# Optimization experiments

Measured on AMD Instinct MI355X. Metric: run time of the kernel, lower is better.

Reference implementation:

```python
import jax, jax.numpy as jnp
import numpy as np

N = 131072          # flattened ray-sample points
C = 32              # output_coordinate_dim per plane
BASE = 128          # base grid resolution
SCALES = [1, 2, 4]  # multiscale_res multipliers
HID = 256           # ResBlock / CondMLP hidden width
OUT = 16            # decoder output dim (geo features)
COMBS = [(0, 1), (0, 2), (1, 2)]  # itertools.combinations(range(3), 2)


def setup_inputs() -> dict:
    key = jax.random.key(0)
    ks = iter(jax.random.split(key, 64))
    inp = {}
    inp['pts'] = jax.random.uniform(next(ks), (N, 3), dtype=jnp.float32)
    inp['aabb'] = jnp.asarray([[0.0, 0.0, 0.0], [1.0, 1.0, 1.0]], dtype=jnp.float32)
    # 9 plane grids: 3 scales x 3 coordinate combinations, uniform in [0.1, 0.5)
    for s, mult in enumerate(SCALES):
        r = BASE * mult
        for ci in range(3):
            inp[f'plane_{s}_{ci}'] = jax.random.uniform(
                next(ks), (C, r, r), dtype=jnp.float32, minval=0.1, maxval=0.5)
    feat_dim = C * len(SCALES)  # concat across scales -> 96
    def lin(k, fin, fout):
        bound = 1.0 / np.sqrt(fin)
        kw, kb = jax.random.split(k)
        w = jax.random.uniform(kw, (fin, fout), dtype=jnp.float32, minval=-bound, maxval=bound)
        b = jax.random.uniform(kb, (fout,), dtype=jnp.float32, minval=-bound, maxval=bound)
        return w, b
    inp['l0_w'], inp['l0_b'] = lin(next(ks), feat_dim, HID)
    # 3 ResBlocks x 3 linears (lz, l1, l2), all 256x256 -> stacked
    rw, rb = [], []
    for _ in range(9):
        w, b = lin(next(ks), HID, HID)
        rw.append(w); rb.append(b)
    inp['res_w'] = jnp.stack(rw).reshape(3, 3, HID, HID)
    inp['res_b'] = jnp.stack(rb).reshape(3, 3, HID)
    inp['l1_w'], inp['l1_b'] = lin(next(ks), HID, OUT)
    return inp


def _bilinear(plane, xy):
    # plane: [C, H, W]; xy: [N, 2] in [-1, 1]; x -> W axis, y -> H axis
    # (F.grid_sample, align_corners=True; border clamp == zeros pad since pts in-bounds)
    Cc, H, W = plane.shape
    x = (xy[:, 0] + 1.0) * 0.5 * (W - 1)
    y = (xy[:, 1] + 1.0) * 0.5 * (H - 1)
    x0 = jnp.clip(jnp.floor(x), 0, W - 2).astype(jnp.int32)
    y0 = jnp.clip(jnp.floor(y), 0, H - 2).astype(jnp.int32)
    x1, y1 = x0 + 1, y0 + 1
    wx = (x - x0)[None, :]
    wy = (y - y0)[None, :]
    v = (plane[:, y0, x0] * (1 - wx) * (1 - wy)
         + plane[:, y0, x1] * wx * (1 - wy)
         + plane[:, y1, x0] * (1 - wx) * wy
         + plane[:, y1, x1] * wx * wy)          # [C, N]
    return v.T                                   # [N, C]


def _interp_ms(xn, planes):
    # planes: list of 3 scales, each a list of 3 [C,H,W] grids
    feats = []
    for scale_planes in planes:
        interp = 1.0
        for plane, (c0, c1) in zip(scale_planes, COMBS):
            xy = jnp.stack([xn[:, c0], xn[:, c1]], axis=-1)
            interp = interp * _bilinear(plane, xy)  # hadamard across planes
        feats.append(interp)
    return jnp.concatenate(feats, axis=-1)          # [N, C*num_scales]


def _cond_mlp(f, l0_w, l0_b, res_w, res_b, l1_w, l1_b):
    x = f @ l0_w + l0_b
    for i in range(3):
        z = jax.nn.relu(x @ res_w[i, 0] + res_b[i, 0])
        res = x + z
        x = jax.nn.relu(res @ res_w[i, 1] + res_b[i, 1])
        x = jax.nn.relu(x @ res_w[i, 2] + res_b[i, 2]) + res
    return jax.nn.sigmoid(x @ l1_w + l1_b)


def reference(pts, aabb,
              plane_0_0, plane_0_1, plane_0_2,
              plane_1_0, plane_1_1, plane_1_2,
              plane_2_0, plane_2_1, plane_2_2,
              l0_w, l0_b, res_w, res_b, l1_w, l1_b):
    xn = (pts - aabb[0]) * (2.0 / (aabb[1] - aabb[0])) - 1.0  # normalize_aabb
    planes = [[plane_0_0, plane_0_1, plane_0_2],
              [plane_1_0, plane_1_1, plane_1_2],
              [plane_2_0, plane_2_1, plane_2_2]]
    feats = _interp_ms(xn, planes)                            # [N, 96]
    return _cond_mlp(feats, l0_w, l0_b, res_w, res_b, l1_w, l1_b)  # [N, 16]
```

## Files before the change

### kernel.cpp

```cpp
#include <hip/hip_runtime.h>

typedef unsigned short u16;
typedef unsigned int u32;
typedef __attribute__((ext_vector_type(2))) unsigned int u32x2;
typedef __attribute__((ext_vector_type(4))) unsigned int u32x4;
typedef __attribute__((ext_vector_type(8))) short short8;
typedef __attribute__((ext_vector_type(8))) _Float16 half8;
typedef __attribute__((ext_vector_type(2))) __fp16 fp16x2;
typedef __attribute__((ext_vector_type(4))) float floatx4;

__device__ __forceinline__ u16 f2h(float f){ _Float16 h = (_Float16)f; return __builtin_bit_cast(u16, h); }
__device__ __forceinline__ u32 pkrtz(float a, float b){
  fp16x2 h = __builtin_amdgcn_cvt_pkrtz(a, b);
  return __builtin_bit_cast(u32, h);
}
__device__ __forceinline__ u32 pkmax0(u32 a){
  u32 d, z = 0;
  asm("v_pk_max_f16 %0, %1, %2" : "=v"(d) : "v"(a), "v"(z));
  return d;
}
__device__ __forceinline__ u32 pkadd(u32 a, u32 b){
  u32 d;
  asm("v_pk_add_f16 %0, %1, %2" : "=v"(d) : "v"(a), "v"(b));
  return d;
}
__device__ __forceinline__ u32 pkmul(u32 a, u32 b){
  u32 d;
  asm("v_pk_mul_f16 %0, %1, %2" : "=v"(d) : "v"(a), "v"(b));
  return d;
}
__device__ __forceinline__ u32 pkfma(u32 a, u32 b, u32 c){
  u32 d;
  asm("v_pk_fma_f16 %0, %1, %2, %3" : "=v"(d) : "v"(a), "v"(b), "v"(c));
  return d;
}

struct PlanePtrs { const void* p[9]; };
struct PtransArgs { const float* src[9]; u16* dst[9]; int blk0[10]; int HW[9]; };

__global__ void ptrans_all_kernel(PtransArgs a){
  __shared__ float tile[32][257];
  int bi = blockIdx.x;
  int i = 0;
  #pragma unroll
  for (int k = 1; k < 9; k++) if (bi >= a.blk0[k]) i = k;
  const float* src = a.src[i];
  u16* dst = a.dst[i];
  const int HW = a.HW[i];
  const int t = threadIdx.x;
  const size_t hw0 = (size_t)(bi - a.blk0[i]) * 256;
  #pragma unroll
  for (int c = 0; c < 32; c++) tile[c][t] = src[(size_t)c*HW + hw0 + t];
  __syncthreads();
  u32* d32 = (u32*)(dst + hw0*32);
  #pragma unroll
  for (int k = 0; k < 16; k++){
    int idx = k*512 + t*2;
    int j = idx >> 5, cc = idx & 31;
    u32 lo = f2h(tile[cc][j]);
    u32 hi = f2h(tile[cc+1][j]);
    d32[k*256 + t] = lo | (hi << 16);
  }
}

__device__ __forceinline__ void wconv_one(const float* src, u16* dst, int fin, int fout, int t){
  int per = fin * fout;
  int m = t / per, r = t - m*per;
  int KS = fin >> 5;
  int e = r & 7;
  int lane = (r >> 3) & 63;
  int fs = r >> 9;
  int ks = fs % KS, ft = fs / KS;
  int of = ft*16 + (lane & 15);
  int k  = ks*32 + (lane >> 4)*8 + e;
  dst[t] = f2h(src[(size_t)m*per + (size_t)k*fout + of]);
}
__global__ void wconv_all_kernel(const float* l0_w, const float* res_w, const float* l1_w,
                                 u16* l0T, u16* resT, u16* l1T){
  int t = blockIdx.x*256 + threadIdx.x;
  if (t < 24576){ wconv_one(l0_w, l0T, 96, 256, t); return; }
  t -= 24576;
  if (t < 589824){ wconv_one(res_w, resT, 256, 256, t); return; }
  t -= 589824;
  if (t < 4096){ wconv_one(l1_w, l1T, 256, 16, t); }
}

__device__ __forceinline__ u32 morton_key(const float* __restrict__ pts,
                                          const float* __restrict__ aabb, int n){
  u32 key = 0;
  #pragma unroll
  for (int d=0; d<3; d++){
    float lo = aabb[d], hi = aabb[3+d];
    float xn = (pts[(size_t)n*3 + d] - lo) * (2.0f/(hi - lo)) - 1.0f;
    int q = (int)((xn + 1.0f) * 8.0f);
    q = q < 0 ? 0 : (q > 15 ? 15 : q);
    #pragma unroll
    for (int b=0; b<4; b++) key |= ((u32)(q >> b) & 1u) << (b*3 + d);
  }
  return key;
}
__global__ void hist_kernel(const float* pts, const float* aabb, u32* hist, int N){
  int n = blockIdx.x*256 + threadIdx.x;
  if (n >= N) return;
  atomicAdd(&hist[morton_key(pts, aabb, n)], 1u);
}
__global__ void scan_kernel(u32* hist){
  __shared__ u32 sums[1024];
  int t = threadIdx.x;
  u32 local[4]; u32 s = 0;
  #pragma unroll
  for (int i=0; i<4; i++){ local[i] = hist[t*4 + i]; s += local[i]; }
  sums[t] = s;
  __syncthreads();
  for (int off=1; off<1024; off<<=1){
    u32 v = (t >= off) ? sums[t-off] : 0;
    __syncthreads();
    sums[t] += v;
    __syncthreads();
  }
  u32 base = (t == 0) ? 0 : sums[t-1];
  #pragma unroll
  for (int i=0; i<4; i++){ u32 c = local[i]; hist[t*4 + i] = base; base += c; }
}
__global__ void scatter_kernel(const float* pts, const float* aabb, u32* hist,
                               int* sidx, int N){
  int n = blockIdx.x*256 + threadIdx.x;
  if (n >= N) return;
  u32 pos = atomicAdd(&hist[morton_key(pts, aabb, n)], 1u);
  sidx[pos] = n;
}

__global__ void interp_fb_kernel(const float* __restrict__ pts, const float* __restrict__ aabb,
                                 PlanePtrs pp, u16* __restrict__ feats, int N)
{
  int n = blockIdx.x*256 + threadIdx.x;
  if (n >= N) return;
  float xn[3];
  #pragma unroll
  for (int d=0; d<3; d++){
    float lo = aabb[d], hi = aabb[3+d];
    xn[d] = (pts[(size_t)n*3 + d] - lo) * (2.0f/(hi - lo)) - 1.0f;
  }
  const int c0s[3] = {0,0,1};
  const int c1s[3] = {1,2,2};
  #pragma unroll
  for (int s=0; s<3; s++){
    const int R = 128 << s;
    float prod[32];
    #pragma unroll
    for (int p=0; p<3; p++){
      float fx = (xn[c0s[p]] + 1.0f) * 0.5f * (float)(R-1);
      float fy = (xn[c1s[p]] + 1.0f) * 0.5f * (float)(R-1);
      float fx0 = fminf(fmaxf(floorf(fx), 0.0f), (float)(R-2));
      float fy0 = fminf(fmaxf(floorf(fy), 0.0f), (float)(R-2));
      int x0 = (int)fx0, y0 = (int)fy0;
      float wx = fx - fx0, wy = fy - fy0;
      float w00 = (1.0f-wx)*(1.0f-wy), w01 = wx*(1.0f-wy);
      float w10 = (1.0f-wx)*wy,        w11 = wx*wy;
      const size_t HW = (size_t)R*R;
      const float* b00f = (const float*)pp.p[s*3+p] + (size_t)y0*R + x0;
      #pragma unroll 4
      for (int c=0; c<32; c++){
        const float* q = b00f + (size_t)c*HW;
        float val = q[0]*w00 + q[1]*w01 + q[R]*w10 + q[R+1]*w11;
        prod[c] = (p == 0) ? val : prod[c]*val;
      }
    }
    #pragma unroll
    for (int vv=0; vv<4; vv++){
      short8 pk8;
      #pragma unroll
      for (int e=0; e<8; e++) pk8[e] = (short)f2h(prod[vv*8+e]);
      *(short8*)(feats + (size_t)n*96 + s*32 + vv*8) = pk8;
    }
  }
}

template<int KSTEPS>
__device__ __forceinline__ void mm_tile(const u16* X, const u16* __restrict__ WTs,
                                        int ftbase, int lane, floatx4 acc[4][4])
{
  const int lr = lane & 15, lg = lane >> 4;
  const u16* wbase = WTs + (size_t)lane*8;
  half8 wc[4];
  #pragma unroll
  for (int rf=0; rf<4; rf++)
    wc[rf] = *(const half8*)(wbase + (size_t)((ftbase+rf)*KSTEPS)*512);
  #pragma unroll 2
  for (int ks=0; ks<KSTEPS; ks++){
    half8 x[4];
    #pragma unroll
    for (int cf=0; cf<4; cf++){
      int pt = cf*16 + lr;
      int byt = (pt*512 + (ks*32 + lg*8)*2) ^ ((pt & 31) << 4);
      x[cf] = *(const half8*)((const char*)X + byt);
    }
    half8 wn[4];
    {
      int ksn = (ks+1 < KSTEPS) ? ks+1 : ks;
      #pragma unroll
      for (int rf=0; rf<4; rf++)
        wn[rf] = *(const half8*)(wbase + (size_t)((ftbase+rf)*KSTEPS + ksn)*512);
    }
    __builtin_amdgcn_s_setprio(1);
    #pragma unroll
    for (int rf=0; rf<4; rf++)
      #pragma unroll
      for (int cf=0; cf<4; cf++)
        acc[rf][cf] = __builtin_amdgcn_mfma_f32_16x16x32_f16(wc[rf], x[cf], acc[rf][cf], 0, 0, 0);
    __builtin_amdgcn_s_setprio(0);
    #pragma unroll
    for (int rf=0; rf<4; rf++) wc[rf] = wn[rf];
  }
}

__device__ __forceinline__ void init_acc(const float* b, int wb, int lg, floatx4 acc[4][4]){
  #pragma unroll
  for (int rf=0; rf<4; rf++){
    float4 v = *(const float4*)(b + wb + rf*16 + lg*4);
    floatx4 bi = (floatx4){v.x, v.y, v.z, v.w};
    #pragma unroll
    for (int cf=0; cf<4; cf++) acc[rf][cf] = bi;
  }
}

template<int MODE>
__global__ __launch_bounds__(256, 3) void mlp_kernel(
    const float* __restrict__ pts, const float* __restrict__ aabb, PlanePtrs pp,
    const u16* __restrict__ feats, const int* __restrict__ sidx,
    const u16* __restrict__ l0T, const u16* __restrict__ resT, const u16* __restrict__ l1T,
    const float* __restrict__ l0_b, const float* __restrict__ res_b, const float* __restrict__ l1_b,
    float* __restrict__ out)
{
  __shared__ u16 X[64*256];
  const int tid = threadIdx.x;
  const int wave = tid >> 6, lane = tid & 63;
  const int lr = lane & 15, lg = lane >> 4;
  int bid = blockIdx.x;
  if constexpr (MODE == 2){
    int nwg = gridDim.x;
    if ((nwg & 7) == 0) bid = (bid & 7)*(nwg >> 3) + (bid >> 3);
  }
  const int n0 = bid * 64;
  const int ftbase = wave * 4;
  const int wb = wave * 64;

  if constexpr (MODE >= 1){
    const int pt = tid >> 2, v = tid & 3;
    const int n = (MODE == 2) ? sidx[n0 + pt] : (n0 + pt);
    float xn[3];
    #pragma unroll
    for (int d=0; d<3; d++){
      float lo = aabb[d], hi = aabb[3+d];
      xn[d] = (pts[(size_t)n*3 + d] - lo) * (2.0f/(hi - lo)) - 1.0f;
    }
    const int c0s[3] = {0,0,1};
    const int c1s[3] = {1,2,2};
    #pragma unroll
    for (int s=0; s<3; s++){
      const int R = 128 << s;
      u32x4 prod;
      #pragma unroll
      for (int p=0; p<3; p++){
        float fx = (xn[c0s[p]] + 1.0f) * 0.5f * (float)(R-1);
        float fy = (xn[c1s[p]] + 1.0f) * 0.5f * (float)(R-1);
        float fx0 = fminf(fmaxf(floorf(fx), 0.0f), (float)(R-2));
        float fy0 = fminf(fmaxf(floorf(fy), 0.0f), (float)(R-2));
        int x0 = (int)fx0, y0 = (int)fy0;
        float wx = fx - fx0, wy = fy - fy0;
        u32 w00p = pkrtz((1.0f-wx)*(1.0f-wy), (1.0f-wx)*(1.0f-wy));
        u32 w01p = pkrtz(wx*(1.0f-wy),        wx*(1.0f-wy));
        u32 w10p = pkrtz((1.0f-wx)*wy,        (1.0f-wx)*wy);
        u32 w11p = pkrtz(wx*wy,               wx*wy);
        const u16* base = (const u16*)pp.p[s*3 + p];
        const u16* b00 = base + ((size_t)y0*R + x0)*32 + v*8;
        const u16* b10 = b00 + (size_t)R*32;
        u32x4 h00 = *(const u32x4*)b00;
        u32x4 h01 = *(const u32x4*)(b00 + 32);
        u32x4 h10 = *(const u32x4*)b10;
        u32x4 h11 = *(const u32x4*)(b10 + 32);
        #pragma unroll
        for (int i=0; i<4; i++){
          u32 a = pkmul(h00[i], w00p);
          a = pkfma(h01[i], w01p, a);
          a = pkfma(h10[i], w10p, a);
          a = pkfma(h11[i], w11p, a);
          prod[i] = (p == 0) ? a : pkmul(prod[i], a);
        }
      }
      int byt = (pt*512 + (s*32 + v*8)*2) ^ ((pt & 31) << 4);
      *(u32x4*)((char*)X + byt) = prod;
    }
  } else {
    #pragma unroll
    for (int i=0; i<3; i++){
      int id = tid + i*256;
      int row = id / 12, sub = id - row*12;
      short8 v = *(const short8*)(feats + (size_t)(n0+row)*96 + sub*8);
      int byt = (row*512 + sub*16) ^ ((row & 31) << 4);
      *(short8*)((char*)X + byt) = v;
    }
  }
  __syncthreads();

  floatx4 acc[4][4];
  u32 pk[4][4][2];

  init_acc(l0_b, wb, lg, acc);
  mm_tile<3>(X, l0T, ftbase, lane, acc);
  __syncthreads();
  #pragma unroll
  for (int rf=0; rf<4; rf++){
    int fby = (wb + rf*16 + lg*4)*2;
    #pragma unroll
    for (int cf=0; cf<4; cf++){
      int pt = cf*16 + lr;
      u32 p0 = pkrtz(acc[rf][cf][0], acc[rf][cf][1]);
      u32 p1 = pkrtz(acc[rf][cf][2], acc[rf][cf][3]);
      pk[rf][cf][0] = p0; pk[rf][cf][1] = p1;
      int byt = (pt*512 + fby) ^ ((pt & 31) << 4);
      *(u32x2*)((char*)X + byt) = (u32x2){p0, p1};
    }
  }
  __syncthreads();

  for (int rb=0; rb<3; rb++){
    const u16* W0 = resT + (size_t)(rb*3+0)*65536;
    const u16* W1 = resT + (size_t)(rb*3+1)*65536;
    const u16* W2 = resT + (size_t)(rb*3+2)*65536;
    const float* b0 = res_b + (rb*3+0)*256;
    const float* b1 = res_b + (rb*3+1)*256;
    const float* b2 = res_b + (rb*3+2)*256;

    init_acc(b0, wb, lg, acc);
    mm_tile<8>(X, W0, ftbase, lane, acc);
    __syncthreads();
    #pragma unroll
    for (int rf=0; rf<4; rf++){
      int fby = (wb + rf*16 + lg*4)*2;
      #pragma unroll
      for (int cf=0; cf<4; cf++){
        int pt = cf*16 + lr;
        u32 p0 = pkadd(pk[rf][cf][0], pkmax0(pkrtz(acc[rf][cf][0], acc[rf][cf][1])));
        u32 p1 = pkadd(pk[rf][cf][1], pkmax0(pkrtz(acc[rf][cf][2], acc[rf][cf][3])));
        pk[rf][cf][0] = p0; pk[rf][cf][1] = p1;
        int byt = (pt*512 + fby) ^ ((pt & 31) << 4);
        *(u32x2*)((char*)X + byt) = (u32x2){p0, p1};
      }
    }
    __syncthreads();

    init_acc(b1, wb, lg, acc);
    mm_tile<8>(X, W1, ftbase, lane, acc);
    __syncthreads();
    #pragma unroll
    for (int rf=0; rf<4; rf++){
      int fby = (wb + rf*16 + lg*4)*2;
      #pragma unroll
      for (int cf=0; cf<4; cf++){
        int pt = cf*16 + lr;
        u32 p0 = pkmax0(pkrtz(acc[rf][cf][0], acc[rf][cf][1]));
        u32 p1 = pkmax0(pkrtz(acc[rf][cf][2], acc[rf][cf][3]));
        int byt = (pt*512 + fby) ^ ((pt & 31) << 4);
        *(u32x2*)((char*)X + byt) = (u32x2){p0, p1};
      }
    }
    __syncthreads();

    init_acc(b2, wb, lg, acc);
    mm_tile<8>(X, W2, ftbase, lane, acc);
    __syncthreads();
    #pragma unroll
    for (int rf=0; rf<4; rf++){
      int fby = (wb + rf*16 + lg*4)*2;
      #pragma unroll
      for (int cf=0; cf<4; cf++){
        int pt = cf*16 + lr;
        u32 p0 = pkadd(pkmax0(pkrtz(acc[rf][cf][0], acc[rf][cf][1])), pk[rf][cf][0]);
        u32 p1 = pkadd(pkmax0(pkrtz(acc[rf][cf][2], acc[rf][cf][3])), pk[rf][cf][1]);
        pk[rf][cf][0] = p0; pk[rf][cf][1] = p1;
        int byt = (pt*512 + fby) ^ ((pt & 31) << 4);
        *(u32x2*)((char*)X + byt) = (u32x2){p0, p1};
      }
    }
    __syncthreads();
  }

  floatx4 accf;
  {
    float4 bo = *(const float4*)(l1_b + lg*4);
    accf = (floatx4){bo.x, bo.y, bo.z, bo.w};
  }
  #pragma unroll 1
  for (int ks=0; ks<8; ks++){
    int pt = wave*16 + lr;
    int byt = (pt*512 + (ks*32 + lg*8)*2) ^ ((pt&31)<<4);
    half8 x = *(const half8*)((const char*)X + byt);
    half8 w = *(const half8*)(l1T + ((size_t)ks*64 + lane)*8);
    accf = __builtin_amdgcn_mfma_f32_16x16x32_f16(w, x, accf, 0, 0, 0);
  }
  {
    int li = n0 + wave*16 + lr;
    int n_out = (MODE == 2) ? sidx[li] : li;
    float4 o;
    o.x = 1.0f / (1.0f + __expf(-accf[0]));
    o.y = 1.0f / (1.0f + __expf(-accf[1]));
    o.z = 1.0f / (1.0f + __expf(-accf[2]));
    o.w = 1.0f / (1.0f + __expf(-accf[3]));
    *(float4*)(out + (size_t)n_out*16 + lg*4) = o;
  }
}

extern "C" void kernel_launch(void* const* d_in, const int* in_sizes, int n_in,
                              void* d_out, int out_size, void* d_ws, size_t ws_size,
                              hipStream_t stream)
{
  const float* pts  = (const float*)d_in[0];
  const float* aabb = (const float*)d_in[1];
  const float* l0_w = (const float*)d_in[11];
  const float* res_w= (const float*)d_in[13];
  const float* l1_w = (const float*)d_in[15];
  const float* l0_b = (const float*)d_in[12];
  const float* res_b= (const float*)d_in[14];
  const float* l1_b = (const float*)d_in[16];
  const int N = in_sizes[0] / 3;

  char* ws = (char*)d_ws;
  const size_t woff_l0  = 0;
  const size_t woff_res = 49152;
  const size_t woff_l1  = woff_res + 9*65536*2;
  const size_t foff     = woff_l1 + 8192;
  const size_t poff     = foff + (size_t)N*96*2;

  static const int HWs[3] = {128*128, 256*256, 512*512};
  size_t pel[9]; size_t tot = 0;
  for (int s=0;s<3;s++) for (int p=0;p<3;p++){ pel[s*3+p] = tot; tot += (size_t)HWs[s]*32; }

  const size_t hoff = (poff + tot*2 + 255) & ~(size_t)255;
  const size_t ioff = hoff + 4096*4;
  const bool tr_mode   = (ws_size >= poff + tot*2);
  const bool sort_mode = (ws_size >= ioff + (size_t)N*4) && ((N/64) % 8 == 0) && (N % 256 == 0);

  wconv_all_kernel<<<(24576+589824+4096+255)/256, 256, 0, stream>>>(
      l0_w, res_w, l1_w, (u16*)(ws+woff_l0), (u16*)(ws+woff_res), (u16*)(ws+woff_l1));

  PlanePtrs pp;
  if (tr_mode){
    u16* pbase = (u16*)(ws + poff);
    PtransArgs pa;
    int b0 = 0;
    for (int i=0;i<9;i++){
      int s = i/3;
      pa.src[i] = (const float*)d_in[2+i];
      pa.dst[i] = pbase + pel[i];
      pa.blk0[i] = b0;
      pa.HW[i] = HWs[s];
      b0 += HWs[s]/256;
      pp.p[i] = pbase + pel[i];
    }
    pa.blk0[9] = b0;
    ptrans_all_kernel<<<b0, 256, 0, stream>>>(pa);

    if (sort_mode){
      u32* hist = (u32*)(ws + hoff);
      int* sidx = (int*)(ws + ioff);
      hipMemsetAsync(hist, 0, 4096*4, stream);
      hist_kernel<<<(N+255)/256, 256, 0, stream>>>(pts, aabb, hist, N);
      scan_kernel<<<1, 1024, 0, stream>>>(hist);
      scatter_kernel<<<(N+255)/256, 256, 0, stream>>>(pts, aabb, hist, sidx, N);
      mlp_kernel<2><<<N/64, 256, 0, stream>>>(pts, aabb, pp, (const u16*)nullptr, sidx,
          (const u16*)(ws+woff_l0), (const u16*)(ws+woff_res), (const u16*)(ws+woff_l1),
          l0_b, res_b, l1_b, (float*)d_out);
    } else {
      mlp_kernel<1><<<N/64, 256, 0, stream>>>(pts, aabb, pp, (const u16*)nullptr, (const int*)nullptr,
          (const u16*)(ws+woff_l0), (const u16*)(ws+woff_res), (const u16*)(ws+woff_l1),
          l0_b, res_b, l1_b, (float*)d_out);
    }
  } else {
    for (int i=0;i<9;i++) pp.p[i] = d_in[2+i];
    interp_fb_kernel<<<(N+255)/256, 256, 0, stream>>>(pts, aabb, pp, (u16*)(ws+foff), N);
    mlp_kernel<0><<<N/64, 256, 0, stream>>>(pts, aabb, pp, (const u16*)(ws+foff), (const int*)nullptr,
        (const u16*)(ws+woff_l0), (const u16*)(ws+woff_res), (const u16*)(ws+woff_l1),
        l0_b, res_b, l1_b, (float*)d_out);
  }
}
```

Baseline: 269.7 us.

## Drop Morton sort path, merge prep kernels, simplify weight loading in MFMA loop

Removes the Morton-order histogram/scan/scatter sorting and the sorted-index indirection in the MLP kernel, so points are processed in natural order. The plane-transpose and weight-conversion kernels are merged into one launch. The MFMA inner loop stops software-prefetching next-step weights and stops unrolling, loading weights in the same step instead. This cuts four launches and the sort overhead, but may lose the gather locality that sorting gave to plane sampling and expose weight-load latency in the GEMM loop.

```diff
diff --git a/kernel.cpp b/kernel.cpp
--- a/kernel.cpp
+++ b/kernel.cpp
@@ -36,32 +36,12 @@
 }
 
 struct PlanePtrs { const void* p[9]; };
-struct PtransArgs { const float* src[9]; u16* dst[9]; int blk0[10]; int HW[9]; };
-
-__global__ void ptrans_all_kernel(PtransArgs a){
-  __shared__ float tile[32][257];
-  int bi = blockIdx.x;
-  int i = 0;
-  #pragma unroll
-  for (int k = 1; k < 9; k++) if (bi >= a.blk0[k]) i = k;
-  const float* src = a.src[i];
-  u16* dst = a.dst[i];
-  const int HW = a.HW[i];
-  const int t = threadIdx.x;
-  const size_t hw0 = (size_t)(bi - a.blk0[i]) * 256;
-  #pragma unroll
-  for (int c = 0; c < 32; c++) tile[c][t] = src[(size_t)c*HW + hw0 + t];
-  __syncthreads();
-  u32* d32 = (u32*)(dst + hw0*32);
-  #pragma unroll
-  for (int k = 0; k < 16; k++){
-    int idx = k*512 + t*2;
-    int j = idx >> 5, cc = idx & 31;
-    u32 lo = f2h(tile[cc][j]);
-    u32 hi = f2h(tile[cc+1][j]);
-    d32[k*256 + t] = lo | (hi << 16);
-  }
-}
+struct PrepArgs {
+  const float* src[9]; u16* dst[9]; int blk0[10]; int HW[9];
+  const float* l0_w; const float* res_w; const float* l1_w;
+  u16* l0T; u16* resT; u16* l1T;
+  int ptrans_blocks;
+};
 
 __device__ __forceinline__ void wconv_one(const float* src, u16* dst, int fin, int fout, int t){
   int per = fin * fout;
@@ -75,59 +55,39 @@
   int k  = ks*32 + (lane >> 4)*8 + e;
   dst[t] = f2h(src[(size_t)m*per + (size_t)k*fout + of]);
 }
-__global__ void wconv_all_kernel(const float* l0_w, const float* res_w, const float* l1_w,
-                                 u16* l0T, u16* resT, u16* l1T){
-  int t = blockIdx.x*256 + threadIdx.x;
-  if (t < 24576){ wconv_one(l0_w, l0T, 96, 256, t); return; }
-  t -= 24576;
-  if (t < 589824){ wconv_one(res_w, resT, 256, 256, t); return; }
-  t -= 589824;
-  if (t < 4096){ wconv_one(l1_w, l1T, 256, 16, t); }
-}
-
-__device__ __forceinline__ u32 morton_key(const float* __restrict__ pts,
-                                          const float* __restrict__ aabb, int n){
-  u32 key = 0;
-  #pragma unroll
-  for (int d=0; d<3; d++){
-    float lo = aabb[d], hi = aabb[3+d];
-    float xn = (pts[(size_t)n*3 + d] - lo) * (2.0f/(hi - lo)) - 1.0f;
-    int q = (int)((xn + 1.0f) * 8.0f);
-    q = q < 0 ? 0 : (q > 15 ? 15 : q);
-    #pragma unroll
-    for (int b=0; b<4; b++) key |= ((u32)(q >> b) & 1u) << (b*3 + d);
-  }
-  return key;
-}
-__global__ void hist_kernel(const float* pts, const float* aabb, u32* hist, int N){
-  int n = blockIdx.x*256 + threadIdx.x;
-  if (n >= N) return;
-  atomicAdd(&hist[morton_key(pts, aabb, n)], 1u);
-}
-__global__ void scan_kernel(u32* hist){
-  __shared__ u32 sums[1024];
-  int t = threadIdx.x;
-  u32 local[4]; u32 s = 0;
-  #pragma unroll
-  for (int i=0; i<4; i++){ local[i] = hist[t*4 + i]; s += local[i]; }
-  sums[t] = s;
-  __syncthreads();
-  for (int off=1; off<1024; off<<=1){
-    u32 v = (t >= off) ? sums[t-off] : 0;
-    __syncthreads();
-    sums[t] += v;
-    __syncthreads();
-  }
-  u32 base = (t == 0) ? 0 : sums[t-1];
-  #pragma unroll
-  for (int i=0; i<4; i++){ u32 c = local[i]; hist[t*4 + i] = base; base += c; }
-}
-__global__ void scatter_kernel(const float* pts, const float* aabb, u32* hist,
-                               int* sidx, int N){
-  int n = blockIdx.x*256 + threadIdx.x;
-  if (n >= N) return;
-  u32 pos = atomicAdd(&hist[morton_key(pts, aabb, n)], 1u);
-  sidx[pos] = n;
+
+__global__ void prep_all_kernel(PrepArgs a){
+  __shared__ float tile[32][257];
+  int bi = blockIdx.x;
+  if (bi < a.ptrans_blocks){
+    int i = 0;
+    #pragma unroll
+    for (int k = 1; k < 9; k++) if (bi >= a.blk0[k]) i = k;
+    const float* src = a.src[i];
+    u16* dst = a.dst[i];
+    const int HW = a.HW[i];
+    const int t = threadIdx.x;
+    const size_t hw0 = (size_t)(bi - a.blk0[i]) * 256;
+    #pragma unroll
+    for (int c = 0; c < 32; c++) tile[c][t] = src[(size_t)c*HW + hw0 + t];
+    __syncthreads();
+    u32* d32 = (u32*)(dst + hw0*32);
+    #pragma unroll
+    for (int k = 0; k < 16; k++){
+      int idx = k*512 + t*2;
+      int j = idx >> 5, cc = idx & 31;
+      u32 lo = f2h(tile[cc][j]);
+      u32 hi = f2h(tile[cc+1][j]);
+      d32[k*256 + t] = lo | (hi << 16);
+    }
+  } else {
+    int t = (bi - a.ptrans_blocks)*256 + threadIdx.x;
+    if (t < 24576){ wconv_one(a.l0_w, a.l0T, 96, 256, t); return; }
+    t -= 24576;
+    if (t < 589824){ wconv_one(a.res_w, a.resT, 256, 256, t); return; }
+    t -= 589824;
+    if (t < 4096){ wconv_one(a.l1_w, a.l1T, 256, 16, t); }
+  }
 }
 
 __global__ void interp_fb_kernel(const float* __restrict__ pts, const float* __restrict__ aabb,
@@ -181,13 +141,12 @@
                                         int ftbase, int lane, floatx4 acc[4][4])
 {
   const int lr = lane & 15, lg = lane >> 4;
-  const u16* wbase = WTs + (size_t)lane*8;
-  half8 wc[4];
-  #pragma unroll
-  for (int rf=0; rf<4; rf++)
-    wc[rf] = *(const half8*)(wbase + (size_t)((ftbase+rf)*KSTEPS)*512);
-  #pragma unroll 2
+  #pragma unroll 1
   for (int ks=0; ks<KSTEPS; ks++){
+    half8 w[4];
+    #pragma unroll
+    for (int rf=0; rf<4; rf++)
+      w[rf] = *(const half8*)(WTs + ((size_t)((ftbase+rf)*KSTEPS + ks)*64 + lane)*8);
     half8 x[4];
     #pragma unroll
     for (int cf=0; cf<4; cf++){
@@ -195,22 +154,13 @@
       int byt = (pt*512 + (ks*32 + lg*8)*2) ^ ((pt & 31) << 4);
       x[cf] = *(const half8*)((const char*)X + byt);
     }
-    half8 wn[4];
-    {
-      int ksn = (ks+1 < KSTEPS) ? ks+1 : ks;
-      #pragma unroll
-      for (int rf=0; rf<4; rf++)
-        wn[rf] = *(const half8*)(wbase + (size_t)((ftbase+rf)*KSTEPS + ksn)*512);
-    }
     __builtin_amdgcn_s_setprio(1);
     #pragma unroll
     for (int rf=0; rf<4; rf++)
       #pragma unroll
       for (int cf=0; cf<4; cf++)
-        acc[rf][cf] = __builtin_amdgcn_mfma_f32_16x16x32_f16(wc[rf], x[cf], acc[rf][cf], 0, 0, 0);
+        acc[rf][cf] = __builtin_amdgcn_mfma_f32_16x16x32_f16(w[rf], x[cf], acc[rf][cf], 0, 0, 0);
     __builtin_amdgcn_s_setprio(0);
-    #pragma unroll
-    for (int rf=0; rf<4; rf++) wc[rf] = wn[rf];
   }
 }
 
@@ -227,7 +177,7 @@
 template<int MODE>
 __global__ __launch_bounds__(256, 3) void mlp_kernel(
     const float* __restrict__ pts, const float* __restrict__ aabb, PlanePtrs pp,
-    const u16* __restrict__ feats, const int* __restrict__ sidx,
+    const u16* __restrict__ feats,
     const u16* __restrict__ l0T, const u16* __restrict__ resT, const u16* __restrict__ l1T,
     const float* __restrict__ l0_b, const float* __restrict__ res_b, const float* __restrict__ l1_b,
     float* __restrict__ out)
@@ -236,18 +186,13 @@
   const int tid = threadIdx.x;
   const int wave = tid >> 6, lane = tid & 63;
   const int lr = lane & 15, lg = lane >> 4;
-  int bid = blockIdx.x;
-  if constexpr (MODE == 2){
-    int nwg = gridDim.x;
-    if ((nwg & 7) == 0) bid = (bid & 7)*(nwg >> 3) + (bid >> 3);
-  }
-  const int n0 = bid * 64;
+  const int n0 = blockIdx.x * 64;
   const int ftbase = wave * 4;
   const int wb = wave * 64;
 
-  if constexpr (MODE >= 1){
+  if constexpr (MODE == 1){
     const int pt = tid >> 2, v = tid & 3;
-    const int n = (MODE == 2) ? sidx[n0 + pt] : (n0 + pt);
+    const int n = n0 + pt;
     float xn[3];
     #pragma unroll
     for (int d=0; d<3; d++){
@@ -400,8 +345,7 @@
     accf = __builtin_amdgcn_mfma_f32_16x16x32_f16(w, x, accf, 0, 0, 0);
   }
   {
-    int li = n0 + wave*16 + lr;
-    int n_out = (MODE == 2) ? sidx[li] : li;
+    int n_out = n0 + wave*16 + lr;
     float4 o;
     o.x = 1.0f / (1.0f + __expf(-accf[0]));
     o.y = 1.0f / (1.0f + __expf(-accf[1]));
@@ -436,18 +380,12 @@
   size_t pel[9]; size_t tot = 0;
   for (int s=0;s<3;s++) for (int p=0;p<3;p++){ pel[s*3+p] = tot; tot += (size_t)HWs[s]*32; }
 
-  const size_t hoff = (poff + tot*2 + 255) & ~(size_t)255;
-  const size_t ioff = hoff + 4096*4;
-  const bool tr_mode   = (ws_size >= poff + tot*2);
-  const bool sort_mode = (ws_size >= ioff + (size_t)N*4) && ((N/64) % 8 == 0) && (N % 256 == 0);
-
-  wconv_all_kernel<<<(24576+589824+4096+255)/256, 256, 0, stream>>>(
-      l0_w, res_w, l1_w, (u16*)(ws+woff_l0), (u16*)(ws+woff_res), (u16*)(ws+woff_l1));
+  const bool tr_mode = (ws_size >= poff + tot*2);
 
   PlanePtrs pp;
   if (tr_mode){
     u16* pbase = (u16*)(ws + poff);
-    PtransArgs pa;
+    PrepArgs pa;
     int b0 = 0;
     for (int i=0;i<9;i++){
       int s = i/3;
@@ -459,28 +397,28 @@
       pp.p[i] = pbase + pel[i];
     }
     pa.blk0[9] = b0;
-    ptrans_all_kernel<<<b0, 256, 0, stream>>>(pa);
-
-    if (sort_mode){
-      u32* hist = (u32*)(ws + hoff);
-      int* sidx = (int*)(ws + ioff);
-      hipMemsetAsync(hist, 0, 4096*4, stream);
-      hist_kernel<<<(N+255)/256, 256, 0, stream>>>(pts, aabb, hist, N);
-      scan_kernel<<<1, 1024, 0, stream>>>(hist);
-      scatter_kernel<<<(N+255)/256, 256, 0, stream>>>(pts, aabb, hist, sidx, N);
-      mlp_kernel<2><<<N/64, 256, 0, stream>>>(pts, aabb, pp, (const u16*)nullptr, sidx,
-          (const u16*)(ws+woff_l0), (const u16*)(ws+woff_res), (const u16*)(ws+woff_l1),
-          l0_b, res_b, l1_b, (float*)d_out);
-    } else {
-      mlp_kernel<1><<<N/64, 256, 0, stream>>>(pts, aabb, pp, (const u16*)nullptr, (const int*)nullptr,
-          (const u16*)(ws+woff_l0), (const u16*)(ws+woff_res), (const u16*)(ws+woff_l1),
-          l0_b, res_b, l1_b, (float*)d_out);
-    }
-  } else {
-    for (int i=0;i<9;i++) pp.p[i] = d_in[2+i];
-    interp_fb_kernel<<<(N+255)/256, 256, 0, stream>>>(pts, aabb, pp, (u16*)(ws+foff), N);
-    mlp_kernel<0><<<N/64, 256, 0, stream>>>(pts, aabb, pp, (const u16*)(ws+foff), (const int*)nullptr,
+    pa.ptrans_blocks = b0;
+    pa.l0_w = l0_w; pa.res_w = res_w; pa.l1_w = l1_w;
+    pa.l0T = (u16*)(ws+woff_l0); pa.resT = (u16*)(ws+woff_res); pa.l1T = (u16*)(ws+woff_l1);
+    const int wconv_blocks = (24576+589824+4096+255)/256;
+    prep_all_kernel<<<b0 + wconv_blocks, 256, 0, stream>>>(pa);
+
+    mlp_kernel<1><<<N/64, 256, 0, stream>>>(pts, aabb, pp, (const u16*)nullptr,
         (const u16*)(ws+woff_l0), (const u16*)(ws+woff_res), (const u16*)(ws+woff_l1),
         l0_b, res_b, l1_b, (float*)d_out);
-  }
-}
+  } else {
+    PrepArgs pa;
+    for (int i=0;i<9;i++){ pa.src[i] = nullptr; pa.dst[i] = nullptr; pa.blk0[i] = 0; pa.HW[i] = HWs[i/3]; pp.p[i] = d_in[2+i]; }
+    pa.blk0[9] = 0;
+    pa.ptrans_blocks = 0;
+    pa.l0_w = l0_w; pa.res_w = res_w; pa.l1_w = l1_w;
+    pa.l0T = (u16*)(ws+woff_l0); pa.resT = (u16*)(ws+woff_res); pa.l1T = (u16*)(ws+woff_l1);
+    const int wconv_blocks = (24576+589824+4096+255)/256;
+    prep_all_kernel<<<wconv_blocks, 256, 0, stream>>>(pa);
+
+    interp_fb_kernel<<<(N+255)/256, 256, 0, stream>>>(pts, aabb, pp, (u16*)(ws+foff), N);
+    mlp_kernel<0><<<N/64, 256, 0, stream>>>(pts, aabb, pp, (const u16*)(ws+foff),
+        (const u16*)(ws+woff_l0), (const u16*)(ws+woff_res), (const u16*)(ws+woff_l1),
+        l0_b, res_b, l1_b, (float*)d_out);
+  }
+}
```

Result: faster. 222.0 us (-17.7%).
